# Performance work log

Measured on AMD Instinct MI355X. Metric: run time of the kernel, lower is better.

The kernel has to match this reference:

```python
import jax, jax.numpy as jnp
import numpy as np

NEG_SLOPE = 0.2   # PyG GATConv default negative_slope
LN_EPS = 1e-5
SOFTMAX_EPS = 1e-16  # PyG softmax denominator eps


def setup_inputs() -> dict:
    key = jax.random.key(0)
    ks = jax.random.split(key, 6)
    N, IN, OUT, H, E = 100000, 128, 64, 2, 1600000
    X = jax.random.normal(ks[0], (N, IN), dtype=jnp.float32)
    edge_index = jax.random.randint(ks[1], (2, E), 0, N, dtype=jnp.int64)
    W = jax.random.normal(ks[2], (H * OUT, IN), dtype=jnp.float32) * 0.05
    att_src = jax.random.normal(ks[3], (H, OUT), dtype=jnp.float32) * 0.05
    att_dst = jax.random.normal(ks[4], (H, OUT), dtype=jnp.float32) * 0.05
    bias = jnp.zeros((OUT,), dtype=jnp.float32)
    ln_gamma = jnp.ones((OUT,), dtype=jnp.float32)
    ln_beta = jnp.zeros((OUT,), dtype=jnp.float32)
    return {"X": X, "edge_index": edge_index, "W": W, "att_src": att_src,
            "att_dst": att_dst, "bias": bias, "ln_gamma": ln_gamma, "ln_beta": ln_beta}


def reference(X, edge_index, W, att_src, att_dst, bias, ln_gamma, ln_beta):
    N = X.shape[0]
    H, F = att_src.shape
    # PyG GATConv default: add self-loops
    loops = jnp.arange(N, dtype=edge_index.dtype)
    src = jnp.concatenate([edge_index[0], loops])  # [Et]
    dst = jnp.concatenate([edge_index[1], loops])  # [Et]
    # linear projection: x' = X @ W^T  -> [N, H, F]
    x = (X @ W.T).reshape(N, H, F)
    # per-node attention logits  [N, H]
    a_src = jnp.einsum('nhf,hf->nh', x, att_src)
    a_dst = jnp.einsum('nhf,hf->nh', x, att_dst)
    # per-edge logits, leaky relu  [Et, H]
    e = jax.nn.leaky_relu(a_src[src] + a_dst[dst], NEG_SLOPE)
    # segment softmax over incoming edges of each dst node
    m = jax.ops.segment_max(e, dst, num_segments=N)          # [N, H]
    ex = jnp.exp(e - m[dst])
    denom = jax.ops.segment_sum(ex, dst, num_segments=N)     # [N, H]
    alpha = ex / (denom[dst] + SOFTMAX_EPS)                  # [Et, H]
    # weighted scatter-add of source features
    msg = x[src] * alpha[:, :, None]                         # [Et, H, F]
    out = jax.ops.segment_sum(msg, dst, num_segments=N)      # [N, H, F]
    # concat=False -> mean over heads, then bias
    out = out.mean(axis=1) + bias                            # [N, F]
    # LayerNorm over features
    mu = out.mean(axis=-1, keepdims=True)
    var = ((out - mu) ** 2).mean(axis=-1, keepdims=True)
    h = (out - mu) * jax.lax.rsqrt(var + LN_EPS) * ln_gamma + ln_beta
    return h
```

## Files before the change

### kernel.cpp

```cpp
#include <hip/hip_runtime.h>
#include <hip/hip_bf16.h>

#define NEG_SLOPE 0.2f
#define LN_EPS 1e-5f
#define SM_EPS 1e-16f

typedef __attribute__((ext_vector_type(8))) short bf16x8;
typedef __attribute__((ext_vector_type(4))) float f32x4;

__device__ inline unsigned short f2bf(float f) {
    unsigned u = __float_as_uint(f);
    return (unsigned short)((u + 0x7FFFu + ((u >> 16) & 1u)) >> 16);
}
__device__ inline float bf_lo(unsigned int v) { return __uint_as_float(v << 16); }
__device__ inline float bf_hi(unsigned int v) { return __uint_as_float(v & 0xffff0000u); }

#define NBIN 512
#define BCAP 4864
#define SCHUNK 4096
#define CURPAD 16

__global__ __launch_bounds__(256) void k_gemm(const float* __restrict__ X,
                                              const float* __restrict__ W,
                                              const float* __restrict__ att_src,
                                              const float* __restrict__ att_dst,
                                              unsigned int* __restrict__ xp,
                                              float2* __restrict__ aS,
                                              float2* __restrict__ aD,
                                              int* __restrict__ binCursor, int N) {
    __shared__ unsigned short Ws[128 * 136];
    __shared__ unsigned short Xs[64 * 136];
    const int t = threadIdx.x;
    const int b0 = blockIdx.x * 64;
    const int lane = t & 63;
    const int w = t >> 6;
    const int c15 = lane & 15;
    const int quad = lane >> 4;

    if (blockIdx.x == 0) {
        for (int i = t; i < NBIN; i += 256) binCursor[i * CURPAD] = i * BCAP;
    }

#pragma unroll
    for (int i = 0; i < 16; ++i) {
        int f = i * 256 + t;
        int nr = f >> 5;
        int q = f & 31;
        float4 v = reinterpret_cast<const float4*>(W)[nr * 32 + q];
        ushort4 b;
        b.x = f2bf(v.x); b.y = f2bf(v.y); b.z = f2bf(v.z); b.w = f2bf(v.w);
        *reinterpret_cast<ushort4*>(&Ws[nr * 136 + q * 4]) = b;
    }
#pragma unroll
    for (int i = 0; i < 8; ++i) {
        int f = i * 256 + t;
        int m = f >> 5;
        int q = f & 31;
        int gr = b0 + m;
        if (gr >= N) gr = N - 1;
        float4 v = reinterpret_cast<const float4*>(X)[(size_t)gr * 32 + q];
        ushort4 b;
        b.x = f2bf(v.x); b.y = f2bf(v.y); b.z = f2bf(v.z); b.w = f2bf(v.w);
        *reinterpret_cast<ushort4*>(&Xs[m * 136 + q * 4]) = b;
    }
    __syncthreads();

    f32x4 acc[8];
#pragma unroll
    for (int ct = 0; ct < 8; ++ct) acc[ct] = (f32x4){0.f, 0.f, 0.f, 0.f};

#pragma unroll
    for (int kc = 0; kc < 4; ++kc) {
        bf16x8 af = *reinterpret_cast<const bf16x8*>(
            &Xs[(w * 16 + c15) * 136 + kc * 32 + quad * 8]);
#pragma unroll
        for (int ct = 0; ct < 8; ++ct) {
            bf16x8 bfr = *reinterpret_cast<const bf16x8*>(
                &Ws[(ct * 16 + c15) * 136 + kc * 32 + quad * 8]);
            acc[ct] = __builtin_amdgcn_mfma_f32_16x16x32_bf16(af, bfr, acc[ct], 0, 0, 0);
        }
    }

    float attS[8], attD[8];
#pragma unroll
    for (int ct = 0; ct < 8; ++ct) {
        attS[ct] = att_src[ct * 16 + c15];
        attD[ct] = att_dst[ct * 16 + c15];
    }

#pragma unroll
    for (int r = 0; r < 4; ++r) {
        int row = b0 + w * 16 + quad * 4 + r;
        float s0 = 0.f, s1 = 0.f, d0 = 0.f, d1 = 0.f;
#pragma unroll
        for (int ct = 0; ct < 4; ++ct) {
            s0 += acc[ct][r] * attS[ct];
            d0 += acc[ct][r] * attD[ct];
            s1 += acc[ct + 4][r] * attS[ct + 4];
            d1 += acc[ct + 4][r] * attD[ct + 4];
        }
#pragma unroll
        for (int o = 1; o < 16; o <<= 1) {
            s0 += __shfl_xor(s0, o);
            s1 += __shfl_xor(s1, o);
            d0 += __shfl_xor(d0, o);
            d1 += __shfl_xor(d1, o);
        }
        if (row < N) {
#pragma unroll
            for (int ct = 0; ct < 4; ++ct) {
                unsigned int p = (unsigned int)f2bf(acc[ct][r]) |
                                 ((unsigned int)f2bf(acc[ct + 4][r]) << 16);
                xp[(size_t)row * 64 + ct * 16 + c15] = p;
            }
            if (c15 == 0) {
                aS[row] = make_float2(s0, s1);
                aD[row] = make_float2(d0, d1);
            }
        }
    }
}

__global__ __launch_bounds__(256) void k_scatter(const int* __restrict__ ei,
                                                 const float2* __restrict__ aS,
                                                 const float2* __restrict__ aD,
                                                 int* __restrict__ binCursor,
                                                 uint2* __restrict__ tmp, int E) {
    __shared__ int off[NBIN];
    const int t = threadIdx.x;
    const int base = blockIdx.x * SCHUNK;

    int se[16], de[16];
    unsigned int ue[16];
#pragma unroll
    for (int k = 0; k < 16; ++k) {
        int i = base + k * 256 + t;
        if (i < E) {
            int s = ei[i];
            int d = ei[E + i];
            se[k] = s; de[k] = d;
            float2 a = aS[s];
            float2 ad2 = aD[d];
            float f0 = a.x + ad2.x; f0 = fmaxf(f0, NEG_SLOPE * f0);
            float f1 = a.y + ad2.y; f1 = fmaxf(f1, NEG_SLOPE * f1);
            ue[k] = (unsigned int)f2bf(__expf(f0)) |
                    ((unsigned int)f2bf(__expf(f1)) << 16);
        } else {
            de[k] = -1;
        }
    }

    for (int i = t; i < NBIN; i += 256) off[i] = 0;
    __syncthreads();
#pragma unroll
    for (int k = 0; k < 16; ++k)
        if (de[k] >= 0) atomicAdd(&off[de[k] >> 8], 1);
    __syncthreads();
    for (int i = t; i < NBIN; i += 256) {
        int h = off[i];
        off[i] = h ? atomicAdd(&binCursor[i * CURPAD], h) : 0;
    }
    __syncthreads();
#pragma unroll
    for (int k = 0; k < 16; ++k) {
        if (de[k] >= 0) {
            int p = atomicAdd(&off[de[k] >> 8], 1);
            tmp[p] = make_uint2(((unsigned)(de[k] & 255) << 24) | (unsigned)se[k],
                                ue[k]);
        }
    }
}

__global__ __launch_bounds__(256) void k_bucket(const uint2* __restrict__ tmp,
                                                const int* __restrict__ binCursor,
                                                const float2* __restrict__ aS,
                                                const float2* __restrict__ aD,
                                                uint2* __restrict__ csr,
                                                unsigned int* __restrict__ rowPtr,
                                                float4* __restrict__ metaN, int N) {
    __shared__ int cnt[256];
    __shared__ int cur[256];
    __shared__ float den0[256], den1[256];
    __shared__ int lds[4];
    const int t = threadIdx.x;
    const int b = blockIdx.x;
    const int start = b * BCAP;
    int m = binCursor[b * CURPAD] - start;
    if (m > BCAP) m = BCAP;

    cnt[t] = 0; den0[t] = 0.f; den1[t] = 0.f;
    __syncthreads();

    for (int k = t; k < m; k += 256) {
        uint2 e = tmp[start + k];
        int li = e.x >> 24;
        atomicAdd(&cnt[li], 1);
        atomicAdd(&den0[li], bf_lo(e.y));
        atomicAdd(&den1[li], bf_hi(e.y));
    }
    __syncthreads();

    int v = cnt[t];
    const int lane = t & 63, w = t >> 6;
    int incl = v;
#pragma unroll
    for (int o = 1; o < 64; o <<= 1) {
        int u = __shfl_up(incl, o);
        if (lane >= o) incl += u;
    }
    if (lane == 63) lds[w] = incl;
    __syncthreads();
    if (t == 0) {
        int run = 0;
        for (int i = 0; i < 4; ++i) { int tv = lds[i]; lds[i] = run; run += tv; }
    }
    __syncthreads();
    int excl = lds[w] + incl - v;
    cur[t] = excl;

    int d = b * 256 + t;
    if (d < N) {
        float2 a = aS[d];
        float2 ad2 = aD[d];
        float f0 = a.x + ad2.x; f0 = fmaxf(f0, NEG_SLOPE * f0);
        float f1 = a.y + ad2.y; f1 = fmaxf(f1, NEG_SLOPE * f1);
        float ws0 = __expf(f0), ws1 = __expf(f1);
        float D0 = den0[t] + ws0, D1 = den1[t] + ws1;
        metaN[d] = make_float4(ws0, ws1,
                               0.5f / (D0 + SM_EPS), 0.5f / (D1 + SM_EPS));
        rowPtr[d] = (unsigned)(start + excl) | ((unsigned)v << 22);
    }
    __syncthreads();

    for (int k = t; k < m; k += 256) {
        uint2 e = tmp[start + k];
        int li = e.x >> 24;
        int p = atomicAdd(&cur[li], 1);
        csr[start + p] = make_uint2(e.x & 0x00FFFFFFu, e.y);
    }
}

__global__ __launch_bounds__(256) void k_agg(const unsigned int* __restrict__ xp,
                                             const float4* __restrict__ metaN,
                                             const unsigned int* __restrict__ rowPtr,
                                             const uint2* __restrict__ csr,
                                             const float* __restrict__ bias,
                                             const float* __restrict__ gamma,
                                             const float* __restrict__ beta,
                                             float* __restrict__ out, int N) {
    const int w = threadIdx.x >> 6, lane = threadIdx.x & 63;
    const int n = blockIdx.x * 4 + w;
    if (n >= N) return;

    float4 meta = metaN[n];
    unsigned int vself = xp[(size_t)n * 64 + lane];
    float S0 = meta.x * bf_lo(vself);
    float S1 = meta.y * bf_hi(vself);

    unsigned int pr = rowPtr[n];
    const int jb = (int)(pr & 0x3FFFFFu);
    const int je = jb + (int)(pr >> 22);
    int j = jb;
    for (; j + 7 < je; j += 8) {
        int ju = __builtin_amdgcn_readfirstlane(j);
        uint2 c[8];
#pragma unroll
        for (int q = 0; q < 8; ++q) c[q] = csr[ju + q];
        unsigned int v[8];
#pragma unroll
        for (int q = 0; q < 8; ++q) v[q] = xp[(size_t)c[q].x * 64 + lane];
#pragma unroll
        for (int q = 0; q < 8; ++q) {
            S0 += bf_lo(c[q].y) * bf_lo(v[q]);
            S1 += bf_hi(c[q].y) * bf_hi(v[q]);
        }
    }
    for (; j + 3 < je; j += 4) {
        int ju = __builtin_amdgcn_readfirstlane(j);
        uint2 c[4];
#pragma unroll
        for (int q = 0; q < 4; ++q) c[q] = csr[ju + q];
        unsigned int v[4];
#pragma unroll
        for (int q = 0; q < 4; ++q) v[q] = xp[(size_t)c[q].x * 64 + lane];
#pragma unroll
        for (int q = 0; q < 4; ++q) {
            S0 += bf_lo(c[q].y) * bf_lo(v[q]);
            S1 += bf_hi(c[q].y) * bf_hi(v[q]);
        }
    }
    for (; j < je; ++j) {
        uint2 c = csr[__builtin_amdgcn_readfirstlane(j)];
        unsigned int vv = xp[(size_t)c.x * 64 + lane];
        S0 += bf_lo(c.y) * bf_lo(vv);
        S1 += bf_hi(c.y) * bf_hi(vv);
    }

    float o = meta.z * S0 + meta.w * S1 + bias[lane];

    float mu = o;
#pragma unroll
    for (int d = 32; d > 0; d >>= 1) mu += __shfl_xor(mu, d);
    mu *= (1.0f / 64.0f);
    float dv = o - mu;
    float var = dv * dv;
#pragma unroll
    for (int d = 32; d > 0; d >>= 1) var += __shfl_xor(var, d);
    var *= (1.0f / 64.0f);
    out[(size_t)n * 64 + lane] = dv * rsqrtf(var + LN_EPS) * gamma[lane] + beta[lane];
}

extern "C" void kernel_launch(void* const* d_in, const int* in_sizes, int n_in,
                              void* d_out, int out_size, void* d_ws, size_t ws_size,
                              hipStream_t stream) {
    const float* X        = (const float*)d_in[0];
    const int*   ei       = (const int*)d_in[1];
    const float* W        = (const float*)d_in[2];
    const float* att_src  = (const float*)d_in[3];
    const float* att_dst  = (const float*)d_in[4];
    const float* bias     = (const float*)d_in[5];
    const float* ln_gamma = (const float*)d_in[6];
    const float* ln_beta  = (const float*)d_in[7];
    float* out = (float*)d_out;

    const int N = in_sizes[0] / 128;
    const int E = in_sizes[1] / 2;
    const int NBUCK = (N + 255) / 256;

    char* ws = (char*)d_ws;
    size_t off = 0;
    auto alloc = [&](size_t bytes) {
        size_t o = off;
        off += (bytes + 255) & ~(size_t)255;
        return o;
    };
    unsigned int* xp     = (unsigned int*)(ws + alloc((size_t)N * 64 * 4));
    float2* aS           = (float2*)(ws + alloc((size_t)N * 8));
    float2* aD           = (float2*)(ws + alloc((size_t)N * 8));
    float4* metaN        = (float4*)(ws + alloc((size_t)N * 16));
    unsigned int* rowPtr = (unsigned int*)(ws + alloc((size_t)N * 4));
    uint2* csr           = (uint2*)(ws + alloc((size_t)NBIN * BCAP * 8));
    uint2* tmp           = (uint2*)(ws + alloc((size_t)NBIN * BCAP * 8));
    int* binCursor       = (int*)(ws + alloc(NBIN * CURPAD * 4));

    k_gemm<<<(N + 63) / 64, 256, 0, stream>>>(X, W, att_src, att_dst, xp, aS, aD,
                                              binCursor, N);
    k_scatter<<<(E + SCHUNK - 1) / SCHUNK, 256, 0, stream>>>(ei, aS, aD,
                                                             binCursor, tmp, E);
    k_bucket<<<NBUCK, 256, 0, stream>>>(tmp, binCursor, aS, aD, csr, rowPtr,
                                        metaN, N);
    k_agg<<<(N + 3) / 4, 256, 0, stream>>>(xp, metaN, rowPtr, csr,
                                           bias, ln_gamma, ln_beta, out, N);
}
```

Measured before the change: 244.4 us.

## Move softmax denominator into aggregation, count degrees with global atomics, prefetch CSR

The per-destination in-degree is now counted with global atomics in the scatter kernel, so the bucket kernel no longer makes its first pass over the binned edges with shared-memory float atomics. The softmax denominator and self-loop weight are now computed inside the aggregation kernel, which sums the edge weights as it reads them, and the metaN buffer is removed. The aggregation loop also prefetches the next 8 CSR entries while gathering features for the current batch. The cost is 1.6M global atomics on a degree array and extra register use in the aggregation kernel.

```diff
diff --git a/kernel.cpp b/kernel.cpp
--- a/kernel.cpp
+++ b/kernel.cpp
@@ -27,7 +27,8 @@
                                               unsigned int* __restrict__ xp,
                                               float2* __restrict__ aS,
                                               float2* __restrict__ aD,
-                                              int* __restrict__ binCursor, int N) {
+                                              int* __restrict__ binCursor,
+                                              int* __restrict__ deg, int N) {
     __shared__ unsigned short Ws[128 * 136];
     __shared__ unsigned short Xs[64 * 136];
     const int t = threadIdx.x;
@@ -39,6 +40,10 @@
 
     if (blockIdx.x == 0) {
         for (int i = t; i < NBIN; i += 256) binCursor[i * CURPAD] = i * BCAP;
+    }
+    if (t < 64) {
+        int gr = b0 + t;
+        if (gr < N) deg[gr] = 0;
     }
 
 #pragma unroll
@@ -125,6 +130,7 @@
                                                  const float2* __restrict__ aS,
                                                  const float2* __restrict__ aD,
                                                  int* __restrict__ binCursor,
+                                                 int* __restrict__ deg,
                                                  uint2* __restrict__ tmp, int E) {
     __shared__ int off[NBIN];
     const int t = threadIdx.x;
@@ -153,8 +159,12 @@
     for (int i = t; i < NBIN; i += 256) off[i] = 0;
     __syncthreads();
 #pragma unroll
-    for (int k = 0; k < 16; ++k)
-        if (de[k] >= 0) atomicAdd(&off[de[k] >> 8], 1);
+    for (int k = 0; k < 16; ++k) {
+        if (de[k] >= 0) {
+            atomicAdd(&off[de[k] >> 8], 1);
+            atomicAdd(&deg[de[k]], 1);
+        }
+    }
     __syncthreads();
     for (int i = t; i < NBIN; i += 256) {
         int h = off[i];
@@ -173,14 +183,11 @@
 
 __global__ __launch_bounds__(256) void k_bucket(const uint2* __restrict__ tmp,
                                                 const int* __restrict__ binCursor,
-                                                const float2* __restrict__ aS,
-                                                const float2* __restrict__ aD,
+                                                const int* __restrict__ deg,
                                                 uint2* __restrict__ csr,
                                                 unsigned int* __restrict__ rowPtr,
-                                                float4* __restrict__ metaN, int N) {
-    __shared__ int cnt[256];
+                                                int N) {
     __shared__ int cur[256];
-    __shared__ float den0[256], den1[256];
     __shared__ int lds[4];
     const int t = threadIdx.x;
     const int b = blockIdx.x;
@@ -188,19 +195,9 @@
     int m = binCursor[b * CURPAD] - start;
     if (m > BCAP) m = BCAP;
 
-    cnt[t] = 0; den0[t] = 0.f; den1[t] = 0.f;
-    __syncthreads();
-
-    for (int k = t; k < m; k += 256) {
-        uint2 e = tmp[start + k];
-        int li = e.x >> 24;
-        atomicAdd(&cnt[li], 1);
-        atomicAdd(&den0[li], bf_lo(e.y));
-        atomicAdd(&den1[li], bf_hi(e.y));
-    }
-    __syncthreads();
-
-    int v = cnt[t];
+    const int d = b * 256 + t;
+    int v = (d < N) ? deg[d] : 0;
+
     const int lane = t & 63, w = t >> 6;
     int incl = v;
 #pragma unroll
@@ -217,19 +214,7 @@
     __syncthreads();
     int excl = lds[w] + incl - v;
     cur[t] = excl;
-
-    int d = b * 256 + t;
-    if (d < N) {
-        float2 a = aS[d];
-        float2 ad2 = aD[d];
-        float f0 = a.x + ad2.x; f0 = fmaxf(f0, NEG_SLOPE * f0);
-        float f1 = a.y + ad2.y; f1 = fmaxf(f1, NEG_SLOPE * f1);
-        float ws0 = __expf(f0), ws1 = __expf(f1);
-        float D0 = den0[t] + ws0, D1 = den1[t] + ws1;
-        metaN[d] = make_float4(ws0, ws1,
-                               0.5f / (D0 + SM_EPS), 0.5f / (D1 + SM_EPS));
-        rowPtr[d] = (unsigned)(start + excl) | ((unsigned)v << 22);
-    }
+    if (d < N) rowPtr[d] = (unsigned)(start + excl) | ((unsigned)v << 22);
     __syncthreads();
 
     for (int k = t; k < m; k += 256) {
@@ -241,7 +226,8 @@
 }
 
 __global__ __launch_bounds__(256) void k_agg(const unsigned int* __restrict__ xp,
-                                             const float4* __restrict__ metaN,
+                                             const float2* __restrict__ aS,
+                                             const float2* __restrict__ aD,
                                              const unsigned int* __restrict__ rowPtr,
                                              const uint2* __restrict__ csr,
                                              const float* __restrict__ bias,
@@ -252,28 +238,50 @@
     const int n = blockIdx.x * 4 + w;
     if (n >= N) return;
 
-    float4 meta = metaN[n];
+    float2 a = aS[n];
+    float2 ad2 = aD[n];
+    float f0 = a.x + ad2.x; f0 = fmaxf(f0, NEG_SLOPE * f0);
+    float f1 = a.y + ad2.y; f1 = fmaxf(f1, NEG_SLOPE * f1);
+    float us0 = __expf(f0), us1 = __expf(f1);
+
     unsigned int vself = xp[(size_t)n * 64 + lane];
-    float S0 = meta.x * bf_lo(vself);
-    float S1 = meta.y * bf_hi(vself);
+    float S0 = us0 * bf_lo(vself);
+    float S1 = us1 * bf_hi(vself);
+    float D0 = us0, D1 = us1;
 
     unsigned int pr = rowPtr[n];
     const int jb = (int)(pr & 0x3FFFFFu);
     const int je = jb + (int)(pr >> 22);
     int j = jb;
-    for (; j + 7 < je; j += 8) {
+    const int nfull = (je - jb) >> 3;
+
+    uint2 cc[8];
+    if (nfull > 0) {
         int ju = __builtin_amdgcn_readfirstlane(j);
-        uint2 c[8];
-#pragma unroll
-        for (int q = 0; q < 8; ++q) c[q] = csr[ju + q];
+#pragma unroll
+        for (int q = 0; q < 8; ++q) cc[q] = csr[ju + q];
+    }
+    for (int bI = 0; bI < nfull; ++bI) {
         unsigned int v[8];
 #pragma unroll
-        for (int q = 0; q < 8; ++q) v[q] = xp[(size_t)c[q].x * 64 + lane];
+        for (int q = 0; q < 8; ++q) v[q] = xp[(size_t)cc[q].x * 64 + lane];
+        uint2 cn[8];
+        {
+            int jn = (bI + 1 < nfull) ? (j + 8) : jb;
+            int ju = __builtin_amdgcn_readfirstlane(jn);
+#pragma unroll
+            for (int q = 0; q < 8; ++q) cn[q] = csr[ju + q];
+        }
 #pragma unroll
         for (int q = 0; q < 8; ++q) {
-            S0 += bf_lo(c[q].y) * bf_lo(v[q]);
-            S1 += bf_hi(c[q].y) * bf_hi(v[q]);
-        }
+            float u0 = bf_lo(cc[q].y), u1 = bf_hi(cc[q].y);
+            D0 += u0; D1 += u1;
+            S0 += u0 * bf_lo(v[q]);
+            S1 += u1 * bf_hi(v[q]);
+        }
+#pragma unroll
+        for (int q = 0; q < 8; ++q) cc[q] = cn[q];
+        j += 8;
     }
     for (; j + 3 < je; j += 4) {
         int ju = __builtin_amdgcn_readfirstlane(j);
@@ -285,18 +293,22 @@
         for (int q = 0; q < 4; ++q) v[q] = xp[(size_t)c[q].x * 64 + lane];
 #pragma unroll
         for (int q = 0; q < 4; ++q) {
-            S0 += bf_lo(c[q].y) * bf_lo(v[q]);
-            S1 += bf_hi(c[q].y) * bf_hi(v[q]);
+            float u0 = bf_lo(c[q].y), u1 = bf_hi(c[q].y);
+            D0 += u0; D1 += u1;
+            S0 += u0 * bf_lo(v[q]);
+            S1 += u1 * bf_hi(v[q]);
         }
     }
     for (; j < je; ++j) {
         uint2 c = csr[__builtin_amdgcn_readfirstlane(j)];
         unsigned int vv = xp[(size_t)c.x * 64 + lane];
-        S0 += bf_lo(c.y) * bf_lo(vv);
-        S1 += bf_hi(c.y) * bf_hi(vv);
-    }
-
-    float o = meta.z * S0 + meta.w * S1 + bias[lane];
+        float u0 = bf_lo(c.y), u1 = bf_hi(c.y);
+        D0 += u0; D1 += u1;
+        S0 += u0 * bf_lo(vv);
+        S1 += u1 * bf_hi(vv);
+    }
+
+    float o = (0.5f / (D0 + SM_EPS)) * S0 + (0.5f / (D1 + SM_EPS)) * S1 + bias[lane];
 
     float mu = o;
 #pragma unroll
@@ -337,18 +349,17 @@
     unsigned int* xp     = (unsigned int*)(ws + alloc((size_t)N * 64 * 4));
     float2* aS           = (float2*)(ws + alloc((size_t)N * 8));
     float2* aD           = (float2*)(ws + alloc((size_t)N * 8));
-    float4* metaN        = (float4*)(ws + alloc((size_t)N * 16));
     unsigned int* rowPtr = (unsigned int*)(ws + alloc((size_t)N * 4));
+    int* deg             = (int*)(ws + alloc((size_t)N * 4));
     uint2* csr           = (uint2*)(ws + alloc((size_t)NBIN * BCAP * 8));
     uint2* tmp           = (uint2*)(ws + alloc((size_t)NBIN * BCAP * 8));
     int* binCursor       = (int*)(ws + alloc(NBIN * CURPAD * 4));
 
     k_gemm<<<(N + 63) / 64, 256, 0, stream>>>(X, W, att_src, att_dst, xp, aS, aD,
-                                              binCursor, N);
+                                              binCursor, deg, N);
     k_scatter<<<(E + SCHUNK - 1) / SCHUNK, 256, 0, stream>>>(ei, aS, aD,
-                                                             binCursor, tmp, E);
-    k_bucket<<<NBUCK, 256, 0, stream>>>(tmp, binCursor, aS, aD, csr, rowPtr,
-                                        metaN, N);
-    k_agg<<<(N + 3) / 4, 256, 0, stream>>>(xp, metaN, rowPtr, csr,
+                                                             binCursor, deg, tmp, E);
+    k_bucket<<<NBUCK, 256, 0, stream>>>(tmp, binCursor, deg, csr, rowPtr, N);
+    k_agg<<<(N + 3) / 4, 256, 0, stream>>>(xp, aS, aD, rowPtr, csr,
                                            bias, ln_gamma, ln_beta, out, N);
 }
```

Result: slower. 281.9 us (+15.4%).
